# Kernel tuning notes

Measured on AMD Instinct MI355X. Metric: run time of the kernel, lower is better.

Reference implementation:

```python
import jax, jax.numpy as jnp
import numpy as np

KS = 3          # deformable kernel size
PAD = 1         # zero padding
N = KS * KS     # sample points per pixel


def conv2d(x, w, b=None, padding=1):
    out = jax.lax.conv_general_dilated(
        x, w, (1, 1), [(padding, padding)] * 2,
        dimension_numbers=('NCHW', 'OIHW', 'NCHW'))
    if b is not None:
        out = out + b[None, :, None, None]
    return out


def setup_inputs() -> dict:
    key = jax.random.key(0)
    k0, k1, k2, k3 = jax.random.split(key, 4)
    B, C, H, W, O = 4, 64, 128, 128, 64
    x = jax.random.normal(k0, (B, C, H, W), jnp.float32)
    # p_conv / m_conv are zero-init in the original; use small random weights
    # so offsets/modulation are non-trivial but sampling stays local.
    w_p = jax.random.normal(k1, (2 * N, C, 3, 3), jnp.float32) * 0.01
    b_p = jnp.zeros((2 * N,), jnp.float32)
    w_m = jax.random.normal(k2, (N, C, 3, 3), jnp.float32) * 0.01
    b_m = jnp.zeros((N,), jnp.float32)
    w_conv = jax.random.normal(k3, (O, C, KS, KS), jnp.float32) / np.sqrt(C * N)
    return {'x': x, 'w_p': w_p, 'b_p': b_p, 'w_m': w_m, 'b_m': b_m, 'w_conv': w_conv}


def reference(x, w_p, b_p, w_m, b_m, w_conv):
    B, C, H, W = x.shape
    offset = conv2d(x, w_p, b_p)              # (B, 2N, H, W): first N rows(x), last N cols(y)
    m = jax.nn.sigmoid(conv2d(x, w_m, b_m))   # (B, N, H, W) modulation
    xp = jnp.pad(x, ((0, 0), (0, 0), (PAD, PAD), (PAD, PAD)))  # zero_padding
    Hp, Wp = H + 2 * PAD, W + 2 * PAD

    # p = p_0 + p_n + offset  (coords in padded image, p_0 starts at 1)
    r = (KS - 1) // 2
    pn_x, pn_y = jnp.meshgrid(jnp.arange(-r, r + 1), jnp.arange(-r, r + 1), indexing='ij')
    pn = jnp.concatenate([pn_x.reshape(-1), pn_y.reshape(-1)]).astype(x.dtype)          # (2N,)
    p0_x, p0_y = jnp.meshgrid(jnp.arange(1, H + 1), jnp.arange(1, W + 1), indexing='ij')
    p0 = jnp.concatenate([jnp.tile(p0_x[None], (N, 1, 1)),
                          jnp.tile(p0_y[None], (N, 1, 1))], 0).astype(x.dtype)           # (2N,H,W)
    p = offset + pn[None, :, None, None] + p0[None]
    p = jnp.moveaxis(p, 1, -1)                # (B,H,W,2N)

    fx = jnp.floor(jax.lax.stop_gradient(p[..., :N]))  # p.detach().floor()
    fy = jnp.floor(jax.lax.stop_gradient(p[..., N:]))
    q_lt_x = jnp.clip(fx, 0, Hp - 1).astype(jnp.int32)
    q_lt_y = jnp.clip(fy, 0, Wp - 1).astype(jnp.int32)
    q_rb_x = jnp.clip(fx + 1, 0, Hp - 1).astype(jnp.int32)
    q_rb_y = jnp.clip(fy + 1, 0, Wp - 1).astype(jnp.int32)
    px = jnp.clip(p[..., :N], 0, Hp - 1)
    py = jnp.clip(p[..., N:], 0, Wp - 1)

    # bilinear kernel weights (same algebra as torch version)
    g_lt = (1 + (q_lt_x - px)) * (1 + (q_lt_y - py))
    g_rb = (1 - (q_rb_x - px)) * (1 - (q_rb_y - py))
    g_lb = (1 + (q_lt_x - px)) * (1 - (q_rb_y - py))
    g_rt = (1 - (q_rb_x - px)) * (1 + (q_lt_y - py))

    xf = xp.reshape(B, C, Hp * Wp)

    def gather(qx, qy):
        idx = (qx * Wp + qy).reshape(B, 1, -1)                      # (B,1,H*W*N)
        return jnp.take_along_axis(xf, idx, axis=2).reshape(B, C, H, W, N)

    x_off = (g_lt[:, None] * gather(q_lt_x, q_lt_y)
             + g_rb[:, None] * gather(q_rb_x, q_rb_y)
             + g_lb[:, None] * gather(q_lt_x, q_rb_y)
             + g_rt[:, None] * gather(q_rb_x, q_lt_y))               # (B,C,H,W,N)

    x_off = x_off * jnp.moveaxis(m, 1, -1)[:, None]                  # modulation (DCNv2)

    # _reshape_x_offset + conv(kernel=ks, stride=ks) == einsum over the N samples
    out = jnp.einsum('bchwk,ock->bohw', x_off,
                     w_conv.reshape(w_conv.shape[0], C, N))
    return out
```

## Files before the change

### kernel.cpp

```cpp
#include <hip/hip_runtime.h>
#include <hip/hip_bf16.h>

#define BB 4
#define CC 64
#define HH 128
#define WW 128
#define OO 64
#define NN 9
#define HW 16384
#define HP 130
#define WP 130

#define WPMB_F  0
#define BPM_OFF 9216
#define WCB_F   9248
#define XT_F    27680

typedef __attribute__((ext_vector_type(8))) short s8v;
typedef __attribute__((ext_vector_type(8))) unsigned short u8v;
typedef __attribute__((ext_vector_type(4))) float f4v;

__device__ __forceinline__ unsigned short f2bu(float f) {
    unsigned int b = __float_as_uint(f);
    return (unsigned short)((b + 0x7FFFu + ((b >> 16) & 1u)) >> 16);
}
__device__ __forceinline__ float bu2f(unsigned short u) {
    return __uint_as_float(((unsigned int)u) << 16);
}

__global__ void k_prep(const float* __restrict__ wp,
                       const float* __restrict__ bp,
                       const float* __restrict__ wm,
                       const float* __restrict__ bm,
                       const float* __restrict__ wcv,
                       float* __restrict__ ws) {
    int tid = blockIdx.x * blockDim.x + threadIdx.x;
    if (tid < 18432) {
        int r = tid / 576;
        int kk = tid % 576;
        int kt = kk >> 6;
        int c = kk & 63;
        int dy = kt / 3, dx = kt % 3;
        float v = 0.f;
        if (r < 18)       v = wp[((r * 64 + c) * 3 + dy) * 3 + dx];
        else if (r < 27)  v = wm[(((r - 18) * 64 + c) * 3 + dy) * 3 + dx];
        ((unsigned short*)(ws + WPMB_F))[tid] = f2bu(v);
    } else if (tid < 18459) {
        int i = tid - 18432;
        ws[BPM_OFF + i] = (i < 18) ? bp[i] : bm[i - 18];
    } else if (tid >= 20480 && tid < 20480 + 36864) {
        int d = tid - 20480;
        int o = d / 576;
        int kk = d % 576;
        int kt = kk >> 6;
        int c = kk & 63;
        ((unsigned short*)(ws + WCB_F))[o * 576 + kk] = f2bu(wcv[(o * 64 + c) * 9 + kt]);
    }
}

__global__ void __launch_bounds__(256) k_xt(const float* __restrict__ x,
                                            float* __restrict__ ws) {
    __shared__ unsigned short tile[64][66];
    int blk = blockIdx.x;
    int b = blk >> 8;
    int hw0 = (blk & 255) * 64;
    int t = threadIdx.x;
    unsigned short* xt = (unsigned short*)(ws + XT_F);

#pragma unroll
    for (int p = 0; p < 16; p++) {
        int c = p * 4 + (t >> 6);
        int i = t & 63;
        tile[c][i] = f2bu(x[((size_t)(b * 64 + c)) * HW + hw0 + i]);
    }
    __syncthreads();
#pragma unroll
    for (int p = 0; p < 16; p++) {
        int i = p * 4 + (t >> 6);
        int c = t & 63;
        xt[((size_t)(b * HW + hw0 + i)) * 64 + c] = tile[c][i];
    }
}

__global__ void __launch_bounds__(256) k_fused(const float* __restrict__ ws,
                                               float* __restrict__ out) {
    __shared__ char ldsbuf[35424];
    unsigned short* halo = (unsigned short*)ldsbuf;
    unsigned short* Sld  = (unsigned short*)ldsbuf;
    unsigned short* A2ld = (unsigned short*)(ldsbuf + 9216);
    float* pm = (float*)(ldsbuf + 28512);

    int t = threadIdx.x;
    int lane = t & 63;
    int wid = t >> 6;
    int ln15 = lane & 15;
    int quad = lane >> 4;

    int blk = blockIdx.x;
    int b = blk >> 8;
    int hw0 = (blk & 255) * 64;
    int h = hw0 >> 7;
    int w0 = hw0 & 127;

    const unsigned short* wpmb = (const unsigned short*)(ws + WPMB_F);
    const unsigned short* wcb  = (const unsigned short*)(ws + WCB_F);
    const unsigned short* xtb  = (const unsigned short*)(ws + XT_F) + (size_t)b * HW * 64;
    const float* bpm = ws + BPM_OFF;

    {
        u8v z = (u8v){0, 0, 0, 0, 0, 0, 0, 0};
#pragma unroll
        for (int i = 0; i < 4; i++) {
            int s = t + i * 256;
            if (s < 792) {
                int cg = s & 3;
                int rc = s >> 2;
                int col = rc % 66;
                int r = rc / 66;
                int h2 = h + r - 1;
                int w2 = w0 + col - 1;
                bool val = ((unsigned)h2 < 128u) && ((unsigned)w2 < 128u);
                u8v e0 = z, e1 = z;
                if (val) {
                    const unsigned short* src = xtb + ((size_t)(h2 * 128 + w2)) * 64 + cg * 16;
                    e0 = *(const u8v*)(src);
                    e1 = *(const u8v*)(src + 8);
                }
                unsigned short* dst = halo + (r * 66 + col) * 72 + cg * 16;
                *(u8v*)(dst) = e0;
                *(u8v*)(dst + 8) = e1;
            }
        }
    }
    __syncthreads();

    f4v acc1[2];
    acc1[0] = (f4v){0.f, 0.f, 0.f, 0.f};
    acc1[1] = (f4v){0.f, 0.f, 0.f, 0.f};

#pragma unroll 1
    for (int kt = 0; kt < 9; kt++) {
        int dy = kt / 3, dx = kt % 3;
#pragma unroll
        for (int ks = 0; ks < 2; ks++) {
            int cs = ks * 32 + quad * 8;
            s8v bf = *(const s8v*)(&halo[(dy * 66 + wid * 16 + ln15 + dx) * 72 + cs]);
#pragma unroll
            for (int mt = 0; mt < 2; mt++) {
                s8v af = *(const s8v*)(wpmb + (mt * 16 + ln15) * 576 + kt * 64 + cs);
                acc1[mt] = __builtin_amdgcn_mfma_f32_16x16x32_bf16(af, bf, acc1[mt], 0, 0, 0);
            }
        }
    }

    {
        int n = wid * 16 + ln15;
        int pw = w0 + n;
#pragma unroll
        for (int mt = 0; mt < 2; mt++) {
#pragma unroll
            for (int r = 0; r < 4; r++) {
                int oc = mt * 16 + quad * 4 + r;
                if (oc < 27) {
                    float v = acc1[mt][r] + bpm[oc];
                    if (oc < 9) {
                        v += (float)(oc / 3 - 1) + (float)(h + 1);
                    } else if (oc < 18) {
                        int k = oc - 9;
                        v += (float)(k % 3 - 1) + (float)(pw + 1);
                    } else {
                        v = 1.f / (1.f + __expf(-v));
                    }
                    pm[oc * 64 + n] = v;
                }
            }
        }
    }
    __syncthreads();

    int p_loc = t >> 2;
    int cq = t & 3;

    f4v acc[4];
#pragma unroll
    for (int mt = 0; mt < 4; mt++) acc[mt] = (f4v){0.f, 0.f, 0.f, 0.f};

#pragma unroll 1
    for (int kt = 0; kt < 9; kt++) {
        float px = pm[kt * 64 + p_loc];
        float py = pm[(9 + kt) * 64 + p_loc];
        float mk = pm[(18 + kt) * 64 + p_loc];

        float fx = floorf(px), fy = floorf(py);
        float pxc = fminf(fmaxf(px, 0.f), (float)(HP - 1));
        float pyc = fminf(fmaxf(py, 0.f), (float)(WP - 1));
        int qltx = (int)fminf(fmaxf(fx, 0.f), (float)(HP - 1));
        int qlty = (int)fminf(fmaxf(fy, 0.f), (float)(WP - 1));
        int qrbx = (int)fminf(fmaxf(fx + 1.f, 0.f), (float)(HP - 1));
        int qrby = (int)fminf(fmaxf(fy + 1.f, 0.f), (float)(WP - 1));

        float gltx = 1.f + ((float)qltx - pxc);
        float glty = 1.f + ((float)qlty - pyc);
        float grbx = 1.f - ((float)qrbx - pxc);
        float grby = 1.f - ((float)qrby - pyc);

        bool vlx = (qltx >= 1) && (qltx <= HH);
        bool vly = (qlty >= 1) && (qlty <= WW);
        bool vrx = (qrbx >= 1) && (qrbx <= HH);
        bool vry = (qrby >= 1) && (qrby <= WW);
        float g0 = (vlx && vly) ? gltx * glty * mk : 0.f;
        float g1 = (vrx && vry) ? grbx * grby * mk : 0.f;
        float g2 = (vlx && vry) ? gltx * grby * mk : 0.f;
        float g3 = (vrx && vly) ? grbx * glty * mk : 0.f;

        int xlt = min(max(qltx - 1, 0), HH - 1);
        int ylt = min(max(qlty - 1, 0), WW - 1);
        int xrb = min(max(qrbx - 1, 0), HH - 1);
        int yrb = min(max(qrby - 1, 0), WW - 1);
        size_t i0 = (size_t)(xlt * WW + ylt) * 64;
        size_t i1 = (size_t)(xrb * WW + yrb) * 64;
        size_t i2 = (size_t)(xlt * WW + yrb) * 64;
        size_t i3 = (size_t)(xrb * WW + ylt) * 64;

        __syncthreads();
        {
            int row = t >> 2, g = t & 3;
            const unsigned short* src = wcb + row * 576 + kt * 64 + g * 16;
            *(u8v*)(&A2ld[row * 72 + g * 16]) = *(const u8v*)(src);
            *(u8v*)(&A2ld[row * 72 + g * 16 + 8]) = *(const u8v*)(src + 8);
        }
        {
            int cbase = cq * 16;
            const unsigned short* s0 = xtb + i0 + cbase;
            const unsigned short* s1 = xtb + i1 + cbase;
            const unsigned short* s2 = xtb + i2 + cbase;
            const unsigned short* s3 = xtb + i3 + cbase;
            u8v e0a = *(const u8v*)(s0), e0b = *(const u8v*)(s0 + 8);
            u8v e1a = *(const u8v*)(s1), e1b = *(const u8v*)(s1 + 8);
            u8v e2a = *(const u8v*)(s2), e2b = *(const u8v*)(s2 + 8);
            u8v e3a = *(const u8v*)(s3), e3b = *(const u8v*)(s3 + 8);
            u8v sva, svb;
#pragma unroll
            for (int j = 0; j < 8; j++) {
                float va = g0 * bu2f(e0a[j]) + g1 * bu2f(e1a[j])
                         + g2 * bu2f(e2a[j]) + g3 * bu2f(e3a[j]);
                float vb = g0 * bu2f(e0b[j]) + g1 * bu2f(e1b[j])
                         + g2 * bu2f(e2b[j]) + g3 * bu2f(e3b[j]);
                sva[j] = f2bu(va);
                svb[j] = f2bu(vb);
            }
            *(u8v*)(&Sld[p_loc * 72 + cbase]) = sva;
            *(u8v*)(&Sld[p_loc * 72 + cbase + 8]) = svb;
        }
        __syncthreads();

#pragma unroll
        for (int ks = 0; ks < 2; ks++) {
            s8v bf = *(const s8v*)(&Sld[(wid * 16 + ln15) * 72 + ks * 32 + quad * 8]);
#pragma unroll
            for (int mt = 0; mt < 4; mt++) {
                s8v af = *(const s8v*)(&A2ld[(mt * 16 + ln15) * 72 + ks * 32 + quad * 8]);
                acc[mt] = __builtin_amdgcn_mfma_f32_16x16x32_bf16(af, bf, acc[mt], 0, 0, 0);
            }
        }
    }

    int pix = hw0 + wid * 16 + ln15;
    float* ob = out + (size_t)b * (OO * HW) + pix;
#pragma unroll
    for (int mt = 0; mt < 4; mt++) {
#pragma unroll
        for (int r = 0; r < 4; r++) {
            ob[(size_t)(mt * 16 + quad * 4 + r) * HW] = acc[mt][r];
        }
    }
}

extern "C" void kernel_launch(void* const* d_in, const int* in_sizes, int n_in,
                              void* d_out, int out_size, void* d_ws, size_t ws_size,
                              hipStream_t stream) {
    const float* x   = (const float*)d_in[0];
    const float* wp  = (const float*)d_in[1];
    const float* bp  = (const float*)d_in[2];
    const float* wm  = (const float*)d_in[3];
    const float* bm  = (const float*)d_in[4];
    const float* wcv = (const float*)d_in[5];
    float* ws = (float*)d_ws;
    float* out = (float*)d_out;

    hipLaunchKernelGGL(k_prep, dim3(224), dim3(256), 0, stream, wp, bp, wm, bm, wcv, ws);
    hipLaunchKernelGGL(k_xt, dim3(1024), dim3(256), 0, stream, x, ws);
    hipLaunchKernelGGL(k_fused, dim3(1024), dim3(256), 0, stream, ws, out);
}
```

Before: 124.5 us.

## Build MFMA operands in registers, dropping LDS staging and per-tap barriers

```diff
diff --git a/kernel.cpp b/kernel.cpp
--- a/kernel.cpp
+++ b/kernel.cpp
@@ -86,8 +86,6 @@
                                                float* __restrict__ out) {
     __shared__ char ldsbuf[35424];
     unsigned short* halo = (unsigned short*)ldsbuf;
-    unsigned short* Sld  = (unsigned short*)ldsbuf;
-    unsigned short* A2ld = (unsigned short*)(ldsbuf + 9216);
     float* pm = (float*)(ldsbuf + 28512);
 
     int t = threadIdx.x;
@@ -178,14 +176,15 @@
     }
     __syncthreads();
 
-    int p_loc = t >> 2;
-    int cq = t & 3;
+    int p_loc = wid * 16 + ln15;
+    int c0 = quad * 8;
+    const unsigned short* wrow = wcb + ln15 * 576 + c0;
 
     f4v acc[4];
 #pragma unroll
     for (int mt = 0; mt < 4; mt++) acc[mt] = (f4v){0.f, 0.f, 0.f, 0.f};
 
-#pragma unroll 1
+#pragma unroll 2
     for (int kt = 0; kt < 9; kt++) {
         float px = pm[kt * 64 + p_loc];
         float py = pm[(9 + kt) * 64 + p_loc];
@@ -217,51 +216,34 @@
         int ylt = min(max(qlty - 1, 0), WW - 1);
         int xrb = min(max(qrbx - 1, 0), HH - 1);
         int yrb = min(max(qrby - 1, 0), WW - 1);
-        size_t i0 = (size_t)(xlt * WW + ylt) * 64;
-        size_t i1 = (size_t)(xrb * WW + yrb) * 64;
-        size_t i2 = (size_t)(xlt * WW + yrb) * 64;
-        size_t i3 = (size_t)(xrb * WW + ylt) * 64;
-
-        __syncthreads();
-        {
-            int row = t >> 2, g = t & 3;
-            const unsigned short* src = wcb + row * 576 + kt * 64 + g * 16;
-            *(u8v*)(&A2ld[row * 72 + g * 16]) = *(const u8v*)(src);
-            *(u8v*)(&A2ld[row * 72 + g * 16 + 8]) = *(const u8v*)(src + 8);
-        }
-        {
-            int cbase = cq * 16;
-            const unsigned short* s0 = xtb + i0 + cbase;
-            const unsigned short* s1 = xtb + i1 + cbase;
-            const unsigned short* s2 = xtb + i2 + cbase;
-            const unsigned short* s3 = xtb + i3 + cbase;
-            u8v e0a = *(const u8v*)(s0), e0b = *(const u8v*)(s0 + 8);
-            u8v e1a = *(const u8v*)(s1), e1b = *(const u8v*)(s1 + 8);
-            u8v e2a = *(const u8v*)(s2), e2b = *(const u8v*)(s2 + 8);
-            u8v e3a = *(const u8v*)(s3), e3b = *(const u8v*)(s3 + 8);
-            u8v sva, svb;
-#pragma unroll
-            for (int j = 0; j < 8; j++) {
-                float va = g0 * bu2f(e0a[j]) + g1 * bu2f(e1a[j])
-                         + g2 * bu2f(e2a[j]) + g3 * bu2f(e3a[j]);
-                float vb = g0 * bu2f(e0b[j]) + g1 * bu2f(e1b[j])
-                         + g2 * bu2f(e2b[j]) + g3 * bu2f(e3b[j]);
-                sva[j] = f2bu(va);
-                svb[j] = f2bu(vb);
-            }
-            *(u8v*)(&Sld[p_loc * 72 + cbase]) = sva;
-            *(u8v*)(&Sld[p_loc * 72 + cbase + 8]) = svb;
-        }
-        __syncthreads();
-
-#pragma unroll
-        for (int ks = 0; ks < 2; ks++) {
-            s8v bf = *(const s8v*)(&Sld[(wid * 16 + ln15) * 72 + ks * 32 + quad * 8]);
-#pragma unroll
-            for (int mt = 0; mt < 4; mt++) {
-                s8v af = *(const s8v*)(&A2ld[(mt * 16 + ln15) * 72 + ks * 32 + quad * 8]);
-                acc[mt] = __builtin_amdgcn_mfma_f32_16x16x32_bf16(af, bf, acc[mt], 0, 0, 0);
-            }
+        const unsigned short* s0 = xtb + (size_t)(xlt * WW + ylt) * 64 + c0;
+        const unsigned short* s1 = xtb + (size_t)(xrb * WW + yrb) * 64 + c0;
+        const unsigned short* s2 = xtb + (size_t)(xlt * WW + yrb) * 64 + c0;
+        const unsigned short* s3 = xtb + (size_t)(xrb * WW + ylt) * 64 + c0;
+
+        u8v e0a = *(const u8v*)(s0), e0b = *(const u8v*)(s0 + 32);
+        u8v e1a = *(const u8v*)(s1), e1b = *(const u8v*)(s1 + 32);
+        u8v e2a = *(const u8v*)(s2), e2b = *(const u8v*)(s2 + 32);
+        u8v e3a = *(const u8v*)(s3), e3b = *(const u8v*)(s3 + 32);
+
+        s8v bf0, bf1;
+#pragma unroll
+        for (int j = 0; j < 8; j++) {
+            float va = g0 * bu2f(e0a[j]) + g1 * bu2f(e1a[j])
+                     + g2 * bu2f(e2a[j]) + g3 * bu2f(e3a[j]);
+            float vb = g0 * bu2f(e0b[j]) + g1 * bu2f(e1b[j])
+                     + g2 * bu2f(e2b[j]) + g3 * bu2f(e3b[j]);
+            bf0[j] = (short)f2bu(va);
+            bf1[j] = (short)f2bu(vb);
+        }
+
+        const unsigned short* wk = wrow + kt * 64;
+#pragma unroll
+        for (int mt = 0; mt < 4; mt++) {
+            s8v af0 = *(const s8v*)(wk + mt * 16 * 576);
+            s8v af1 = *(const s8v*)(wk + mt * 16 * 576 + 32);
+            acc[mt] = __builtin_amdgcn_mfma_f32_16x16x32_bf16(af0, bf0, acc[mt], 0, 0, 0);
+            acc[mt] = __builtin_amdgcn_mfma_f32_16x16x32_bf16(af1, bf1, acc[mt], 0, 0, 0);
         }
     }
 
```

New measurement: 166.6 us. 1.34x slower.

## Swap MFMA tiling so each wave owns output channels and double-buffer samples

Applied to the files above, without the earlier changes.

```diff
diff --git a/kernel.cpp b/kernel.cpp
--- a/kernel.cpp
+++ b/kernel.cpp
@@ -82,12 +82,12 @@
     }
 }
 
-__global__ void __launch_bounds__(256) k_fused(const float* __restrict__ ws,
-                                               float* __restrict__ out) {
+__global__ void __launch_bounds__(256, 3) k_fused(const float* __restrict__ ws,
+                                                  float* __restrict__ out) {
     __shared__ char ldsbuf[35424];
     unsigned short* halo = (unsigned short*)ldsbuf;
-    unsigned short* Sld  = (unsigned short*)ldsbuf;
-    unsigned short* A2ld = (unsigned short*)(ldsbuf + 9216);
+    unsigned short* Sbuf0 = (unsigned short*)ldsbuf;
+    unsigned short* Sbuf1 = (unsigned short*)(ldsbuf + 8960);
     float* pm = (float*)(ldsbuf + 28512);
 
     int t = threadIdx.x;
@@ -183,7 +183,9 @@
 
     f4v acc[4];
 #pragma unroll
-    for (int mt = 0; mt < 4; mt++) acc[mt] = (f4v){0.f, 0.f, 0.f, 0.f};
+    for (int nt = 0; nt < 4; nt++) acc[nt] = (f4v){0.f, 0.f, 0.f, 0.f};
+
+    const unsigned short* wrow = wcb + (wid * 16 + ln15) * 576 + quad * 8;
 
 #pragma unroll 1
     for (int kt = 0; kt < 9; kt++) {
@@ -222,13 +224,7 @@
         size_t i2 = (size_t)(xlt * WW + yrb) * 64;
         size_t i3 = (size_t)(xrb * WW + ylt) * 64;
 
-        __syncthreads();
-        {
-            int row = t >> 2, g = t & 3;
-            const unsigned short* src = wcb + row * 576 + kt * 64 + g * 16;
-            *(u8v*)(&A2ld[row * 72 + g * 16]) = *(const u8v*)(src);
-            *(u8v*)(&A2ld[row * 72 + g * 16 + 8]) = *(const u8v*)(src + 8);
-        }
+        unsigned short* Sw = (kt & 1) ? Sbuf1 : Sbuf0;
         {
             int cbase = cq * 16;
             const unsigned short* s0 = xtb + i0 + cbase;
@@ -249,29 +245,31 @@
                 sva[j] = f2bu(va);
                 svb[j] = f2bu(vb);
             }
-            *(u8v*)(&Sld[p_loc * 72 + cbase]) = sva;
-            *(u8v*)(&Sld[p_loc * 72 + cbase + 8]) = svb;
+            *(u8v*)(&Sw[p_loc * 70 + cbase]) = sva;
+            *(u8v*)(&Sw[p_loc * 70 + cbase + 8]) = svb;
         }
         __syncthreads();
 
-#pragma unroll
-        for (int ks = 0; ks < 2; ks++) {
-            s8v bf = *(const s8v*)(&Sld[(wid * 16 + ln15) * 72 + ks * 32 + quad * 8]);
-#pragma unroll
-            for (int mt = 0; mt < 4; mt++) {
-                s8v af = *(const s8v*)(&A2ld[(mt * 16 + ln15) * 72 + ks * 32 + quad * 8]);
-                acc[mt] = __builtin_amdgcn_mfma_f32_16x16x32_bf16(af, bf, acc[mt], 0, 0, 0);
-            }
-        }
-    }
-
-    int pix = hw0 + wid * 16 + ln15;
-    float* ob = out + (size_t)b * (OO * HW) + pix;
-#pragma unroll
-    for (int mt = 0; mt < 4; mt++) {
+        const unsigned short* wk = wrow + kt * 64;
+        s8v af0 = *(const s8v*)(wk);
+        s8v af1 = *(const s8v*)(wk + 32);
+#pragma unroll
+        for (int nt = 0; nt < 4; nt++) {
+            s8v bf0 = *(const s8v*)(&Sw[(nt * 16 + ln15) * 70 + quad * 8]);
+            s8v bf1 = *(const s8v*)(&Sw[(nt * 16 + ln15) * 70 + 32 + quad * 8]);
+            acc[nt] = __builtin_amdgcn_mfma_f32_16x16x32_bf16(af0, bf0, acc[nt], 0, 0, 0);
+            acc[nt] = __builtin_amdgcn_mfma_f32_16x16x32_bf16(af1, bf1, acc[nt], 0, 0, 0);
+        }
+    }
+
+    float* ob = out + (size_t)b * (OO * HW);
+    int mrow = wid * 16 + quad * 4;
+#pragma unroll
+    for (int nt = 0; nt < 4; nt++) {
+        int pix = hw0 + nt * 16 + ln15;
 #pragma unroll
         for (int r = 0; r < 4; r++) {
-            ob[(size_t)(mt * 16 + quad * 4 + r) * HW] = acc[mt][r];
+            ob[(size_t)(mrow + r) * HW + pix] = acc[nt][r];
         }
     }
 }
```

New measurement: 148.2 us. 1.19x slower.
